# Performance work log

Measured on AMD Instinct MI355X. Metric: run time of the kernel, lower is better.

Reference implementation:

```python
import jax, jax.numpy as jnp
import numpy as np

B, C, T = 64, 22, 2560
U0, U1 = 128, 64  # lstm units per direction


def _lstm(x, Wx, Wh, b, reverse):
    """Keras-style LSTM. x:[B,T,D]. Returns (seq:[B,T,U], last:[B,U])."""
    if reverse:
        x = x[:, ::-1, :]
    U = Wh.shape[0]
    # precompute input projections for all timesteps: [T,B,4U]
    xz = (jnp.einsum('btd,dk->btk', x, Wx) + b).transpose(1, 0, 2)
    h0 = jnp.zeros((x.shape[0], U), x.dtype)
    c0 = jnp.zeros((x.shape[0], U), x.dtype)

    def step(carry, z):
        h, c = carry
        z = z + h @ Wh
        i = jax.nn.sigmoid(z[:, :U])
        f = jax.nn.sigmoid(z[:, U:2 * U])
        g = jnp.tanh(z[:, 2 * U:3 * U])
        o = jax.nn.sigmoid(z[:, 3 * U:])
        c = f * c + i * g
        h = o * jnp.tanh(c)
        return (h, c), h

    (h_last, _), hs = jax.lax.scan(step, (h0, c0), xz)
    hs = hs.transpose(1, 0, 2)  # [B,T,U]
    if reverse:
        hs = hs[:, ::-1, :]
    return hs, h_last


def setup_inputs() -> dict:
    key = jax.random.key(0)
    ks = jax.random.split(key, 20)
    s = 0.05
    d = {"x": jax.random.normal(ks[0], (B, C, T), jnp.float32)}
    # layer 0 (input dim C=22, units U0), fwd + bwd
    d["l0f_Wx"] = jax.random.normal(ks[1], (C, 4 * U0)) * s
    d["l0f_Wh"] = jax.random.normal(ks[2], (U0, 4 * U0)) * s
    d["l0f_b"] = jnp.zeros((4 * U0,))
    d["l0b_Wx"] = jax.random.normal(ks[3], (C, 4 * U0)) * s
    d["l0b_Wh"] = jax.random.normal(ks[4], (U0, 4 * U0)) * s
    d["l0b_b"] = jnp.zeros((4 * U0,))
    # layer 1 (input dim 2*U0=256, units U1), fwd + bwd
    d["l1f_Wx"] = jax.random.normal(ks[5], (2 * U0, 4 * U1)) * s
    d["l1f_Wh"] = jax.random.normal(ks[6], (U1, 4 * U1)) * s
    d["l1f_b"] = jnp.zeros((4 * U1,))
    d["l1b_Wx"] = jax.random.normal(ks[7], (2 * U0, 4 * U1)) * s
    d["l1b_Wh"] = jax.random.normal(ks[8], (U1, 4 * U1)) * s
    d["l1b_b"] = jnp.zeros((4 * U1,))
    # dense head: 2*U1=128 -> 128 -> 64 -> 1
    d["d0_W"] = jax.random.normal(ks[9], (2 * U1, 128)) * s
    d["d0_b"] = jnp.zeros((128,))
    d["d1_W"] = jax.random.normal(ks[10], (128, 64)) * s
    d["d1_b"] = jnp.zeros((64,))
    d["out_W"] = jax.random.normal(ks[11], (64, 1)) * s
    d["out_b"] = jnp.zeros((1,))
    return d


def reference(x, l0f_Wx, l0f_Wh, l0f_b, l0b_Wx, l0b_Wh, l0b_b,
              l1f_Wx, l1f_Wh, l1f_b, l1b_Wx, l1b_Wh, l1b_b,
              d0_W, d0_b, d1_W, d1_b, out_W, out_b):
    h = x.transpose(0, 2, 1)  # [B,T,C]
    # BiLSTM 0, return_sequences=True
    f_seq, _ = _lstm(h, l0f_Wx, l0f_Wh, l0f_b, reverse=False)
    b_seq, _ = _lstm(h, l0b_Wx, l0b_Wh, l0b_b, reverse=True)
    h = jnp.concatenate([f_seq, b_seq], axis=-1)  # [B,T,2*U0]
    # BiLSTM 1, return last state
    _, f_last = _lstm(h, l1f_Wx, l1f_Wh, l1f_b, reverse=False)
    _, b_last = _lstm(h, l1b_Wx, l1b_Wh, l1b_b, reverse=True)
    h = jnp.concatenate([f_last, b_last], axis=-1)  # [B,2*U1]
    # dense head (dropout inactive at inference)
    h = jax.nn.relu(h @ d0_W + d0_b)
    h = jax.nn.relu(h @ d1_W + d1_b)
    return jax.nn.sigmoid(h @ out_W + out_b)  # [B,1]
```

## Files before the change

### kernel.cpp

```cpp
#include <hip/hip_runtime.h>
#include <stdint.h>

#define TT 2560
#define BB 64
#define CC 22

typedef unsigned short ushort_t;
typedef __attribute__((ext_vector_type(4))) float floatx4;
typedef __attribute__((ext_vector_type(8))) short bf16x8;
typedef __attribute__((ext_vector_type(4))) int intx4;

__device__ __forceinline__ float bf2f(ushort_t u){
  union { uint32_t i; float f; } v; v.i = ((uint32_t)u) << 16; return v.f;
}
__device__ __forceinline__ ushort_t f2bf(float f){
  union { float f; uint32_t i; } v; v.f = f;
  uint32_t r = v.i + 0x7FFFu + ((v.i >> 16) & 1u);
  return (ushort_t)(r >> 16);
}
__device__ __forceinline__ float fsig(float x){ return 1.f/(1.f + __expf(-x)); }
__device__ __forceinline__ float ftanh(float x){ return 2.f/(1.f + __expf(-2.f*x)) - 1.f; }

__device__ __forceinline__ void ldsbar(){
  asm volatile("s_waitcnt lgkmcnt(0)\n\ts_barrier" ::: "memory");
}

__global__ __launch_bounds__(256) void k_convert_x(const float* __restrict__ x, ushort_t* __restrict__ xc){
  int i4 = blockIdx.x*256 + threadIdx.x;
  if (i4 >= BB*CC*TT/4) return;
  const float4 v = ((const float4*)x)[i4];
  uint2 o;
  o.x = (uint32_t)f2bf(v.x) | ((uint32_t)f2bf(v.y) << 16);
  o.y = (uint32_t)f2bf(v.z) | ((uint32_t)f2bf(v.w) << 16);
  ((uint2*)xc)[i4] = o;
}

__global__ __launch_bounds__(256) void k_prep_xa(const ushort_t* __restrict__ xc, ushort_t* __restrict__ xA){
  int idx = blockIdx.x*256 + threadIdx.x;
  if (idx >= 16*TT*16) return;
  int l16 = idx & 15;
  int rest = idx >> 4;
  int t = rest % TT, cb = rest / TT;
  int c4 = l16 >> 2, q = l16 & 3;
  int b = cb*4 + c4;
  ushort_t v[8];
  #pragma unroll
  for (int j=0;j<8;j++){
    int c = q*8 + j;
    v[j] = (c < CC) ? xc[((size_t)b*CC + c)*TT + t] : (ushort_t)0;
  }
  *(uint4*)(xA + (size_t)idx*8) = *(const uint4*)v;
}

__global__ __launch_bounds__(256) void k_wmax(const float* __restrict__ w0f, const float* __restrict__ w0b,
                                              const float* __restrict__ w1f, const float* __restrict__ w1b,
                                              float* __restrict__ scl){
  const int b = blockIdx.x;
  const float* W = (b==0) ? w0f : (b==1) ? w0b : (b==2) ? w1f : w1b;
  const int n = (b < 2) ? 128*512 : 64*256;
  float mx = 0.f;
  for (int i = threadIdx.x; i < n; i += 256) mx = fmaxf(mx, fabsf(W[i]));
  __shared__ float red[256];
  red[threadIdx.x] = mx;
  __syncthreads();
  for (int s = 128; s > 0; s >>= 1){
    if (threadIdx.x < s) red[threadIdx.x] = fmaxf(red[threadIdx.x], red[threadIdx.x+s]);
    __syncthreads();
  }
  if (threadIdx.x == 0) scl[b] = fmaxf(red[0], 1e-8f);
}

__global__ __launch_bounds__(256) void k_prep_l0(const float* __restrict__ WxF, const float* __restrict__ WhF,
                                                 const float* __restrict__ WxB, const float* __restrict__ WhB,
                                                 const float* __restrict__ scl,
                                                 char* __restrict__ W0Q, ushort_t* __restrict__ B0X){
  int idx = blockIdx.x*256 + threadIdx.x;
  if (idx >= 2*512*160) return;
  int dir = idx / 81920; int r = idx % 81920; int n = r / 160; int k = r % 160;
  if (k < 128){
    const float* Wh = dir ? WhB : WhF;
    float sw = scl[dir];
    W0Q[(size_t)dir*65536 + n*128 + k] = (char)(int)rintf(Wh[k*512 + n] * (127.f/sw));
  } else {
    const float* Wx = dir ? WxB : WxF;
    int kx = k - 128;
    float v = (kx < CC) ? Wx[kx*512 + n] : 0.f;
    B0X[(size_t)dir*16384 + n*32 + kx] = f2bf(v);
  }
}

__global__ __launch_bounds__(256) void k_prep_l1(const float* __restrict__ WhF, const float* __restrict__ WhB,
                                                 const float* __restrict__ scl,
                                                 char* __restrict__ W1Q){
  int idx = blockIdx.x*256 + threadIdx.x;
  if (idx >= 2*256*64) return;
  int dir = idx >> 14; int r = idx & 16383; int n = r >> 6; int k = r & 63;
  const float* Wh = dir ? WhB : WhF;
  float sw = scl[2+dir];
  W1Q[(size_t)dir*16384 + n*64 + k] = (char)(int)rintf(Wh[k*256 + n] * (127.f/sw));
}

__global__ __launch_bounds__(256) void k_prep_wxT(const float* __restrict__ Wf, const float* __restrict__ Wb,
                                                  ushort_t* __restrict__ WT){
  int idx = blockIdx.x*256 + threadIdx.x;
  int dir = idx >> 16; int r = idx & 65535; int n = r >> 8; int k = r & 255;
  const float* W = dir ? Wb : Wf;
  WT[idx] = f2bf(W[k*256 + n]);
}

__global__ __launch_bounds__(512, 2) void k_lstm0m(
  const ushort_t* __restrict__ xA, const char* __restrict__ W0Q,
  const ushort_t* __restrict__ B0X, const float* __restrict__ scl,
  const float* __restrict__ bF, const float* __restrict__ bB,
  ushort_t* __restrict__ h0seq)
{
  const int dir = blockIdx.x & 1, cb = blockIdx.x >> 1;
  const int tid = threadIdx.x;
  const int wv = tid >> 6, lane = tid & 63, m = lane & 15, q = lane >> 4;
  const int u = wv*16 + m;
  const float* bi = dir ? bB : bF;
  const float sclc = scl[dir] * (1.f/16129.f);

  __shared__ __align__(16) char AbufC[2][4][144];

  bf16x8 Bfx[4];
  intx4  BfQ[4][2];
  {
    const ushort_t* Bx = B0X + (size_t)dir*16384;
    const char*     Bq = W0Q + (size_t)dir*65536;
    #pragma unroll
    for (int g=0; g<4; g++){
      int nrow = (g*8 + wv)*16 + m;
      Bfx[g] = *(const bf16x8*)(Bx + (size_t)nrow*32 + q*8);
      #pragma unroll
      for (int kt=0; kt<2; kt++)
        BfQ[g][kt] = *(const intx4*)(Bq + (size_t)nrow*128 + kt*64 + q*16);
    }
  }
  float bz[4];
  #pragma unroll
  for (int g=0; g<4; g++) bz[g] = bi[g*128 + u];

  if (tid < (int)(sizeof(AbufC)/4)) ((uint32_t*)AbufC)[tid] = 0u;

  const ushort_t* xap = xA + (((size_t)cb*TT)*16 + (size_t)((m>>2)*4 + q))*8;
  uint4 px[4];
  #pragma unroll
  for (int j=0; j<4; j++){
    int tj = dir ? (TT-1-j) : j;
    px[j] = *(const uint4*)(xap + (size_t)tj*128);
  }
  const ushort_t* xpp = xap + (size_t)(dir ? (TT-5) : 4)*128;
  const int xstep = dir ? -128 : 128;
  __syncthreads();

  const floatx4 z4 = {0.f,0.f,0.f,0.f};
  const intx4  zi = {0,0,0,0};
  float cst = 0.f;
  const int t00 = dir ? TT-1 : 0;
  ushort_t* hp = h0seq + ((size_t)(cb*4 + q)*TT + t00)*256 + dir*128 + u;
  const int hstep = dir ? -256 : 256;

  const int ch = m >> 2;

  for (int i = 0; i < TT/4; ++i){
    #pragma unroll
    for (int p = 0; p < 4; ++p){
      const int s = i*4 + p;
      const int cur = s & 1, nxt = cur ^ 1;

      const char* ar = &AbufC[cur][ch][0];
      intx4 AfQ0 = *(const intx4*)(ar + q*16);
      intx4 AfQ1 = *(const intx4*)(ar + 64 + q*16);
      bf16x8 Ax = *(const bf16x8*)&px[p];

      floatx4 ax0 = __builtin_amdgcn_mfma_f32_16x16x32_bf16(Ax, Bfx[0], z4, 0,0,0);
      floatx4 ax1 = __builtin_amdgcn_mfma_f32_16x16x32_bf16(Ax, Bfx[1], z4, 0,0,0);
      floatx4 ax2 = __builtin_amdgcn_mfma_f32_16x16x32_bf16(Ax, Bfx[2], z4, 0,0,0);
      floatx4 ax3 = __builtin_amdgcn_mfma_f32_16x16x32_bf16(Ax, Bfx[3], z4, 0,0,0);

      intx4 aq0 = __builtin_amdgcn_mfma_i32_16x16x64_i8(AfQ0, BfQ[0][0], zi, 0,0,0);
      intx4 aq1 = __builtin_amdgcn_mfma_i32_16x16x64_i8(AfQ0, BfQ[1][0], zi, 0,0,0);
      intx4 aq2 = __builtin_amdgcn_mfma_i32_16x16x64_i8(AfQ0, BfQ[2][0], zi, 0,0,0);
      intx4 aq3 = __builtin_amdgcn_mfma_i32_16x16x64_i8(AfQ0, BfQ[3][0], zi, 0,0,0);
      aq0 = __builtin_amdgcn_mfma_i32_16x16x64_i8(AfQ1, BfQ[0][1], aq0, 0,0,0);
      aq1 = __builtin_amdgcn_mfma_i32_16x16x64_i8(AfQ1, BfQ[1][1], aq1, 0,0,0);
      aq2 = __builtin_amdgcn_mfma_i32_16x16x64_i8(AfQ1, BfQ[2][1], aq2, 0,0,0);
      aq3 = __builtin_amdgcn_mfma_i32_16x16x64_i8(AfQ1, BfQ[3][1], aq3, 0,0,0);

      px[p] = *(const uint4*)xpp;
      xpp += xstep;

      {
        float ig = fsig ((float)aq0[0]*sclc + ax0[0] + bz[0]);
        float fg = fsig ((float)aq1[0]*sclc + ax1[0] + bz[1]);
        float gg = ftanh((float)aq2[0]*sclc + ax2[0] + bz[2]);
        float og = fsig ((float)aq3[0]*sclc + ax3[0] + bz[3]);
        float cc = fg*cst + ig*gg;
        cst = cc;
        float hf = og*ftanh(cc);
        AbufC[nxt][q][u] = (char)(int)rintf(hf * 127.f);
        *hp = f2bf(hf); hp += hstep;
      }
      ldsbar();
    }
  }
}

__global__ __launch_bounds__(512) void k_xz1_gemm(const ushort_t* __restrict__ h0seq,
                                                  const ushort_t* __restrict__ WxT,
                                                  ushort_t* __restrict__ xz1)
{
  const int mb  = blockIdx.x;
  const int dir = blockIdx.y;
  const ushort_t* W   = WxT + (size_t)dir*256*256;
  ushort_t*       out = xz1 + (size_t)dir*BB*TT*256;
  const int wave = threadIdx.x >> 6;
  const int lane = threadIdx.x & 63;
  const int mw = wave & 3;
  const int nw = wave >> 2;
  const int m_ = lane & 15;
  const int q_ = lane >> 4;

  floatx4 acc[2][8];
  #pragma unroll
  for (int a=0;a<2;a++)
    #pragma unroll
    for (int n=0;n<8;n++) acc[a][n] = (floatx4)0.f;

  const size_t Abase = ((size_t)mb*128 + mw*32 + m_)*256 + q_*8;
  const size_t Bbase = ((size_t)nw*128 + m_)*256 + q_*8;

  for (int kc = 0; kc < 256; kc += 32){
    bf16x8 afr[2];
    #pragma unroll
    for (int mt=0;mt<2;mt++)
      afr[mt] = *(const bf16x8*)(h0seq + Abase + (size_t)mt*16*256 + kc);
    #pragma unroll
    for (int nt=0;nt<8;nt++){
      bf16x8 bfr = *(const bf16x8*)(W + Bbase + (size_t)nt*16*256 + kc);
      #pragma unroll
      for (int mt=0;mt<2;mt++)
        acc[mt][nt] = __builtin_amdgcn_mfma_f32_16x16x32_bf16(afr[mt], bfr, acc[mt][nt], 0,0,0);
    }
  }
  #pragma unroll
  for (int mt=0;mt<2;mt++)
    #pragma unroll
    for (int r=0;r<4;r++){
      size_t bt = (size_t)mb*128 + mw*32 + mt*16 + q_*4 + r;
      ushort_t* rowp = out + bt*256;
      #pragma unroll
      for (int wvz=0; wvz<4; wvz++){
        uint32_t lo = f2bf(acc[mt][wvz][r]);
        uint32_t hi = f2bf(acc[mt][wvz+4][r]);
        *(uint32_t*)(rowp + (wvz*16+m_)*4 + 2*nw) = lo | (hi << 16);
      }
    }
}

__global__ __launch_bounds__(256, 1) void k_lstm1m(
  const ushort_t* __restrict__ xz1R,
  const char* __restrict__ W1Q,
  const float* __restrict__ scl,
  const float* __restrict__ bF, const float* __restrict__ bB,
  float* __restrict__ h1last)
{
  const int dir = blockIdx.x & 1, cb = blockIdx.x >> 1;
  const int tid = threadIdx.x;
  const int wv = tid >> 6, lane = tid & 63, m = lane & 15, q = lane >> 4;
  const int u = wv*16 + m;
  const float* bi = dir ? bB : bF;
  const float sclc = scl[2+dir] * (1.f/16129.f);

  __shared__ __align__(16) char HbufC[2][4][80];

  intx4 BfQ[4];
  {
    const char* Bq = W1Q + (size_t)dir*16384;
    #pragma unroll
    for (int g=0; g<4; g++){
      int nrow = (g*4 + wv)*16 + m;
      BfQ[g] = *(const intx4*)(Bq + (size_t)nrow*64 + q*16);
    }
  }
  float bz[4];
  #pragma unroll
  for (int g=0; g<4; g++) bz[g] = bi[g*64 + u];

  if (tid < (int)(sizeof(HbufC)/4)) ((uint32_t*)HbufC)[tid] = 0u;

  const ushort_t* xzr = xz1R + ((size_t)dir*BB + (size_t)(cb*4+q))*TT*256 + (size_t)u*4;
  uint2 pz[4];
  #pragma unroll
  for (int j=0; j<4; j++){
    int tj = dir ? (TT-1-j) : j;
    pz[j] = *(const uint2*)(xzr + (size_t)tj*256);
  }
  const ushort_t* xpp = xzr + (size_t)(dir ? (TT-5) : 4)*256;
  const int zstep = dir ? -256 : 256;
  __syncthreads();

  const intx4 zi = {0,0,0,0};
  float cst = 0.f, hl = 0.f;
  const int ch = m >> 2;

  for (int i = 0; i < TT/4; ++i){
    #pragma unroll
    for (int p = 0; p < 4; ++p){
      const int s = i*4 + p;
      const int cur = s & 1, nxt = cur ^ 1;

      intx4 AfQ = *(const intx4*)(&HbufC[cur][ch][0] + q*16);

      float w0 = bz[0] + bf2f((ushort_t)(pz[p].x & 0xffff));
      float w1 = bz[1] + bf2f((ushort_t)(pz[p].x >> 16));
      float w2 = bz[2] + bf2f((ushort_t)(pz[p].y & 0xffff));
      float w3 = bz[3] + bf2f((ushort_t)(pz[p].y >> 16));
      pz[p] = *(const uint2*)xpp;
      xpp += zstep;

      intx4 a0 = __builtin_amdgcn_mfma_i32_16x16x64_i8(AfQ, BfQ[0], zi, 0,0,0);
      intx4 a1 = __builtin_amdgcn_mfma_i32_16x16x64_i8(AfQ, BfQ[1], zi, 0,0,0);
      intx4 a2 = __builtin_amdgcn_mfma_i32_16x16x64_i8(AfQ, BfQ[2], zi, 0,0,0);
      intx4 a3 = __builtin_amdgcn_mfma_i32_16x16x64_i8(AfQ, BfQ[3], zi, 0,0,0);

      {
        float ig = fsig((float)a0[0]*sclc + w0);
        float fg = fsig((float)a1[0]*sclc + w1);
        float gg = ftanh((float)a2[0]*sclc + w2);
        float og = fsig((float)a3[0]*sclc + w3);
        float cc = fg*cst + ig*gg;
        cst = cc;
        hl = og*ftanh(cc);
        HbufC[nxt][q][u] = (char)(int)rintf(hl * 127.f);
      }
      ldsbar();
    }
  }
  h1last[(size_t)(cb*4 + q)*128 + dir*64 + u] = hl;
}

__global__ __launch_bounds__(128) void k_head(
  const float* __restrict__ h1last,
  const float* __restrict__ d0W, const float* __restrict__ d0b,
  const float* __restrict__ d1W, const float* __restrict__ d1b,
  const float* __restrict__ oW,  const float* __restrict__ ob,
  float* __restrict__ outp)
{
  const int b = blockIdx.x;
  const int j = threadIdx.x;
  __shared__ float v0[128], v1[128];
  v0[j] = h1last[b*128 + j];
  __syncthreads();
  float acc = d0b[j];
  #pragma unroll
  for (int k=0;k<128;k++) acc += v0[k]*d0W[k*128 + j];
  v1[j] = fmaxf(acc, 0.f);
  __syncthreads();
  if (j < 64){
    float a2 = d1b[j];
    #pragma unroll
    for (int k=0;k<128;k++) a2 += v1[k]*d1W[k*64 + j];
    float p = fmaxf(a2, 0.f) * oW[j];
    #pragma unroll
    for (int off=32; off>0; off>>=1) p += __shfl_down(p, off, 64);
    if (j == 0) outp[b] = 1.f/(1.f + __expf(-(p + ob[0])));
  }
}

extern "C" void kernel_launch(void* const* d_in, const int* in_sizes, int n_in,
                              void* d_out, int out_size, void* d_ws, size_t ws_size,
                              hipStream_t stream)
{
  const float* x     = (const float*)d_in[0];
  const float* l0fWx = (const float*)d_in[1];
  const float* l0fWh = (const float*)d_in[2];
  const float* l0fb  = (const float*)d_in[3];
  const float* l0bWx = (const float*)d_in[4];
  const float* l0bWh = (const float*)d_in[5];
  const float* l0bb  = (const float*)d_in[6];
  const float* l1fWx = (const float*)d_in[7];
  const float* l1fWh = (const float*)d_in[8];
  const float* l1fb  = (const float*)d_in[9];
  const float* l1bWx = (const float*)d_in[10];
  const float* l1bWh = (const float*)d_in[11];
  const float* l1bb  = (const float*)d_in[12];
  const float* d0W = (const float*)d_in[13];
  const float* d0b = (const float*)d_in[14];
  const float* d1W = (const float*)d_in[15];
  const float* d1b = (const float*)d_in[16];
  const float* oW  = (const float*)d_in[17];
  const float* ob  = (const float*)d_in[18];
  float* outp = (float*)d_out;

  char* ws = (char*)d_ws;
  const size_t OFF_XT  = 0;
  const size_t OFF_SCL = 7208960ull;
  const size_t OFF_H0  = OFF_XT  + 7864320ull;
  const size_t OFF_XZ  = OFF_H0  + 83886080ull;
  const size_t OFF_XA  = OFF_XZ;
  const size_t OFF_WT  = OFF_XZ  + 167772160ull;
  const size_t OFF_B0  = OFF_WT  + 262144ull;
  const size_t OFF_B0X = OFF_B0  + 131072ull;
  const size_t OFF_B1  = OFF_B0  + 327680ull;
  const size_t OFF_H1  = OFF_B1  + 65536ull;

  ushort_t* xc  = (ushort_t*)(ws + OFF_XT);
  float*    sclp= (float*)(ws + OFF_SCL);
  ushort_t* h0  = (ushort_t*)(ws + OFF_H0);
  ushort_t* xz1 = (ushort_t*)(ws + OFF_XZ);
  ushort_t* xA  = (ushort_t*)(ws + OFF_XA);
  ushort_t* WT  = (ushort_t*)(ws + OFF_WT);
  char*     W0Q = (char*)(ws + OFF_B0);
  ushort_t* B0X = (ushort_t*)(ws + OFF_B0X);
  char*     W1Q = (char*)(ws + OFF_B1);
  float*    h1l = (float*)(ws + OFF_H1);

  hipLaunchKernelGGL(k_convert_x,   dim3(3520), dim3(256), 0, stream, x, xc);
  hipLaunchKernelGGL(k_prep_xa,     dim3(2560), dim3(256), 0, stream, xc, xA);
  hipLaunchKernelGGL(k_wmax,        dim3(4),    dim3(256), 0, stream, l0fWh, l0bWh, l1fWh, l1bWh, sclp);
  hipLaunchKernelGGL(k_prep_l0,     dim3(640),  dim3(256), 0, stream, l0fWx, l0fWh, l0bWx, l0bWh, sclp, W0Q, B0X);
  hipLaunchKernelGGL(k_prep_l1,     dim3(128),  dim3(256), 0, stream, l1fWh, l1bWh, sclp, W1Q);
  hipLaunchKernelGGL(k_prep_wxT,    dim3(512),  dim3(256), 0, stream, l1fWx, l1bWx, WT);
  hipLaunchKernelGGL(k_lstm0m,      dim3(32),   dim3(512), 0, stream, xA, W0Q, B0X, sclp, l0fb, l0bb, h0);
  hipLaunchKernelGGL(k_xz1_gemm,    dim3(1280,2), dim3(512), 0, stream, h0, WT, xz1);
  hipLaunchKernelGGL(k_lstm1m,      dim3(32),   dim3(256), 0, stream, xz1, W1Q, sclp, l1fb, l1bb, h1l);
  hipLaunchKernelGGL(k_head,        dim3(64),   dim3(128), 0, stream,
                     h1l, d0W, d0b, d1W, d1b, oW, ob, outp);
}
```

Measured before the change: 2.514 ms.

## Run layer-1 LSTM with one wave per batch/direction, dropping block barriers

```diff
diff --git a/kernel.cpp b/kernel.cpp
--- a/kernel.cpp
+++ b/kernel.cpp
@@ -23,6 +23,9 @@
 
 __device__ __forceinline__ void ldsbar(){
   asm volatile("s_waitcnt lgkmcnt(0)\n\ts_barrier" ::: "memory");
+}
+__device__ __forceinline__ void ldsfence(){
+  asm volatile("s_waitcnt lgkmcnt(0)" ::: "memory");
 }
 
 __global__ __launch_bounds__(256) void k_convert_x(const float* __restrict__ x, ushort_t* __restrict__ xc){
@@ -259,38 +262,39 @@
     }
 }
 
-__global__ __launch_bounds__(256, 1) void k_lstm1m(
+__global__ __launch_bounds__(64, 1) void k_lstm1m(
   const ushort_t* __restrict__ xz1R,
   const char* __restrict__ W1Q,
   const float* __restrict__ scl,
   const float* __restrict__ bF, const float* __restrict__ bB,
   float* __restrict__ h1last)
 {
-  const int dir = blockIdx.x & 1, cb = blockIdx.x >> 1;
-  const int tid = threadIdx.x;
-  const int wv = tid >> 6, lane = tid & 63, m = lane & 15, q = lane >> 4;
-  const int u = wv*16 + m;
+  const int dir = blockIdx.x & 1, b = blockIdx.x >> 1;
+  const int lane = threadIdx.x;
+  const int m = lane & 15, q = lane >> 4;
+  const int u = q*16 + m;
   const float* bi = dir ? bB : bF;
   const float sclc = scl[2+dir] * (1.f/16129.f);
-
-  __shared__ __align__(16) char HbufC[2][4][80];
-
-  intx4 BfQ[4];
+  const bool qodd = (q & 1), qhi = (q >= 2);
+
+  __shared__ __align__(16) char hbuf[128];
+
+  intx4 BfQ[4][4];
   {
     const char* Bq = W1Q + (size_t)dir*16384;
     #pragma unroll
-    for (int g=0; g<4; g++){
-      int nrow = (g*4 + wv)*16 + m;
-      BfQ[g] = *(const intx4*)(Bq + (size_t)nrow*64 + q*16);
-    }
+    for (int g=0; g<4; g++)
+      #pragma unroll
+      for (int ut=0; ut<4; ut++)
+        BfQ[g][ut] = *(const intx4*)(Bq + (size_t)(g*64 + ut*16 + m)*64 + q*16);
   }
   float bz[4];
   #pragma unroll
   for (int g=0; g<4; g++) bz[g] = bi[g*64 + u];
 
-  if (tid < (int)(sizeof(HbufC)/4)) ((uint32_t*)HbufC)[tid] = 0u;
-
-  const ushort_t* xzr = xz1R + ((size_t)dir*BB + (size_t)(cb*4+q))*TT*256 + (size_t)u*4;
+  if (lane < 32) ((uint32_t*)hbuf)[lane] = 0u;
+
+  const ushort_t* xzr = xz1R + ((size_t)dir*BB + b)*TT*256 + (size_t)u*4;
   uint2 pz[4];
   #pragma unroll
   for (int j=0; j<4; j++){
@@ -299,19 +303,15 @@
   }
   const ushort_t* xpp = xzr + (size_t)(dir ? (TT-5) : 4)*256;
   const int zstep = dir ? -256 : 256;
-  __syncthreads();
+  ldsfence();
 
   const intx4 zi = {0,0,0,0};
   float cst = 0.f, hl = 0.f;
-  const int ch = m >> 2;
 
   for (int i = 0; i < TT/4; ++i){
     #pragma unroll
     for (int p = 0; p < 4; ++p){
-      const int s = i*4 + p;
-      const int cur = s & 1, nxt = cur ^ 1;
-
-      intx4 AfQ = *(const intx4*)(&HbufC[cur][ch][0] + q*16);
+      intx4 AfQ = *(const intx4*)(hbuf + q*16);
 
       float w0 = bz[0] + bf2f((ushort_t)(pz[p].x & 0xffff));
       float w1 = bz[1] + bf2f((ushort_t)(pz[p].x >> 16));
@@ -320,25 +320,32 @@
       pz[p] = *(const uint2*)xpp;
       xpp += zstep;
 
-      intx4 a0 = __builtin_amdgcn_mfma_i32_16x16x64_i8(AfQ, BfQ[0], zi, 0,0,0);
-      intx4 a1 = __builtin_amdgcn_mfma_i32_16x16x64_i8(AfQ, BfQ[1], zi, 0,0,0);
-      intx4 a2 = __builtin_amdgcn_mfma_i32_16x16x64_i8(AfQ, BfQ[2], zi, 0,0,0);
-      intx4 a3 = __builtin_amdgcn_mfma_i32_16x16x64_i8(AfQ, BfQ[3], zi, 0,0,0);
+      intx4 C[4][4];
+      #pragma unroll
+      for (int g=0; g<4; g++)
+        #pragma unroll
+        for (int ut=0; ut<4; ut++)
+          C[g][ut] = __builtin_amdgcn_mfma_i32_16x16x64_i8(AfQ, BfQ[g][ut], zi, 0,0,0);
+
+      int z0i = qhi ? (qodd ? C[0][3][0] : C[0][2][0]) : (qodd ? C[0][1][0] : C[0][0][0]);
+      int z1i = qhi ? (qodd ? C[1][3][0] : C[1][2][0]) : (qodd ? C[1][1][0] : C[1][0][0]);
+      int z2i = qhi ? (qodd ? C[2][3][0] : C[2][2][0]) : (qodd ? C[2][1][0] : C[2][0][0]);
+      int z3i = qhi ? (qodd ? C[3][3][0] : C[3][2][0]) : (qodd ? C[3][1][0] : C[3][0][0]);
 
       {
-        float ig = fsig((float)a0[0]*sclc + w0);
-        float fg = fsig((float)a1[0]*sclc + w1);
-        float gg = ftanh((float)a2[0]*sclc + w2);
-        float og = fsig((float)a3[0]*sclc + w3);
+        float ig = fsig((float)z0i*sclc + w0);
+        float fg = fsig((float)z1i*sclc + w1);
+        float gg = ftanh((float)z2i*sclc + w2);
+        float og = fsig((float)z3i*sclc + w3);
         float cc = fg*cst + ig*gg;
         cst = cc;
         hl = og*ftanh(cc);
-        HbufC[nxt][q][u] = (char)(int)rintf(hl * 127.f);
+        hbuf[u] = (char)(int)rintf(hl * 127.f);
       }
-      ldsbar();
+      ldsfence();
     }
   }
-  h1last[(size_t)(cb*4 + q)*128 + dir*64 + u] = hl;
+  h1last[(size_t)b*128 + dir*64 + u] = hl;
 }
 
 __global__ __launch_bounds__(128) void k_head(
@@ -425,7 +432,7 @@
   hipLaunchKernelGGL(k_prep_wxT,    dim3(512),  dim3(256), 0, stream, l1fWx, l1bWx, WT);
   hipLaunchKernelGGL(k_lstm0m,      dim3(32),   dim3(512), 0, stream, xA, W0Q, B0X, sclp, l0fb, l0bb, h0);
   hipLaunchKernelGGL(k_xz1_gemm,    dim3(1280,2), dim3(512), 0, stream, h0, WT, xz1);
-  hipLaunchKernelGGL(k_lstm1m,      dim3(32),   dim3(256), 0, stream, xz1, W1Q, sclp, l1fb, l1bb, h1l);
+  hipLaunchKernelGGL(k_lstm1m,      dim3(128),  dim3(64), 0, stream, xz1, W1Q, sclp, l1fb, l1bb, h1l);
   hipLaunchKernelGGL(k_head,        dim3(64),   dim3(128), 0, stream,
                      h1l, d0W, d0b, d1W, d1b, oW, ob, outp);
 }
```

New measurement: 2.737 ms. 1.09x slower.

## Split layer-0 LSTM to one batch row per block with gate-per-lane activation

Applied to the files above, without the earlier changes.

```diff
diff --git a/kernel.cpp b/kernel.cpp
--- a/kernel.cpp
+++ b/kernel.cpp
@@ -37,12 +37,10 @@
 
 __global__ __launch_bounds__(256) void k_prep_xa(const ushort_t* __restrict__ xc, ushort_t* __restrict__ xA){
   int idx = blockIdx.x*256 + threadIdx.x;
-  if (idx >= 16*TT*16) return;
-  int l16 = idx & 15;
-  int rest = idx >> 4;
-  int t = rest % TT, cb = rest / TT;
-  int c4 = l16 >> 2, q = l16 & 3;
-  int b = cb*4 + c4;
+  if (idx >= BB*TT*4) return;
+  int q = idx & 3;
+  int rest = idx >> 2;
+  int t = rest % TT, b = rest / TT;
   ushort_t v[8];
   #pragma unroll
   for (int j=0;j<8;j++){
@@ -76,16 +74,19 @@
                                                  char* __restrict__ W0Q, ushort_t* __restrict__ B0X){
   int idx = blockIdx.x*256 + threadIdx.x;
   if (idx >= 2*512*160) return;
-  int dir = idx / 81920; int r = idx % 81920; int n = r / 160; int k = r % 160;
+  int dir = idx / 81920; int r0 = idx % 81920; int n = r0 / 160; int k = r0 % 160;
+  int g = n >> 7, u = n & 127;
+  int wv = u >> 4, qq = (u >> 2) & 3, r = u & 3;
+  int row = (qq*8 + wv)*16 + (r*4 + g);
   if (k < 128){
     const float* Wh = dir ? WhB : WhF;
     float sw = scl[dir];
-    W0Q[(size_t)dir*65536 + n*128 + k] = (char)(int)rintf(Wh[k*512 + n] * (127.f/sw));
+    W0Q[(size_t)dir*65536 + row*128 + k] = (char)(int)rintf(Wh[k*512 + n] * (127.f/sw));
   } else {
     const float* Wx = dir ? WxB : WxF;
     int kx = k - 128;
     float v = (kx < CC) ? Wx[kx*512 + n] : 0.f;
-    B0X[(size_t)dir*16384 + n*32 + kx] = f2bf(v);
+    B0X[(size_t)dir*16384 + row*32 + kx] = f2bf(v);
   }
 }
 
@@ -108,20 +109,25 @@
   WT[idx] = f2bf(W[k*256 + n]);
 }
 
-__global__ __launch_bounds__(512, 2) void k_lstm0m(
+__global__ __launch_bounds__(512, 1) void k_lstm0m(
   const ushort_t* __restrict__ xA, const char* __restrict__ W0Q,
   const ushort_t* __restrict__ B0X, const float* __restrict__ scl,
   const float* __restrict__ bF, const float* __restrict__ bB,
   ushort_t* __restrict__ h0seq)
 {
-  const int dir = blockIdx.x & 1, cb = blockIdx.x >> 1;
+  const int dir = blockIdx.x & 1, b = blockIdx.x >> 1;
   const int tid = threadIdx.x;
   const int wv = tid >> 6, lane = tid & 63, m = lane & 15, q = lane >> 4;
-  const int u = wv*16 + m;
+  const int g  = m & 3;
+  const int u  = wv*16 + q*4 + (m >> 2);
   const float* bi = dir ? bB : bF;
   const float sclc = scl[dir] * (1.f/16129.f);
-
-  __shared__ __align__(16) char AbufC[2][4][144];
+  const float em = (g==2) ? -2.f : -1.f;
+  const float ym = (g==2) ?  2.f :  1.f;
+  const float ya = (g==2) ? -1.f :  0.f;
+  const float bzl = bi[g*128 + u];
+
+  __shared__ __align__(16) char AbufC[2][128];
 
   bf16x8 Bfx[4];
   intx4  BfQ[4][2];
@@ -129,39 +135,34 @@
     const ushort_t* Bx = B0X + (size_t)dir*16384;
     const char*     Bq = W0Q + (size_t)dir*65536;
     #pragma unroll
-    for (int g=0; g<4; g++){
-      int nrow = (g*8 + wv)*16 + m;
-      Bfx[g] = *(const bf16x8*)(Bx + (size_t)nrow*32 + q*8);
+    for (int qt=0; qt<4; qt++){
+      int nrow = (qt*8 + wv)*16 + m;
+      Bfx[qt] = *(const bf16x8*)(Bx + (size_t)nrow*32 + q*8);
       #pragma unroll
       for (int kt=0; kt<2; kt++)
-        BfQ[g][kt] = *(const intx4*)(Bq + (size_t)nrow*128 + kt*64 + q*16);
-    }
-  }
-  float bz[4];
-  #pragma unroll
-  for (int g=0; g<4; g++) bz[g] = bi[g*128 + u];
-
-  if (tid < (int)(sizeof(AbufC)/4)) ((uint32_t*)AbufC)[tid] = 0u;
-
-  const ushort_t* xap = xA + (((size_t)cb*TT)*16 + (size_t)((m>>2)*4 + q))*8;
+        BfQ[qt][kt] = *(const intx4*)(Bq + (size_t)nrow*128 + kt*64 + q*16);
+    }
+  }
+
+  if (tid < 64) ((uint32_t*)AbufC)[tid] = 0u;
+
+  const ushort_t* xap = xA + ((size_t)b*TT*4 + q)*8;
   uint4 px[4];
   #pragma unroll
   for (int j=0; j<4; j++){
     int tj = dir ? (TT-1-j) : j;
-    px[j] = *(const uint4*)(xap + (size_t)tj*128);
-  }
-  const ushort_t* xpp = xap + (size_t)(dir ? (TT-5) : 4)*128;
-  const int xstep = dir ? -128 : 128;
+    px[j] = *(const uint4*)(xap + (size_t)tj*32);
+  }
+  const ushort_t* xpp = xap + (size_t)(dir ? (TT-5) : 4)*32;
+  const int xstep = dir ? -32 : 32;
   __syncthreads();
 
   const floatx4 z4 = {0.f,0.f,0.f,0.f};
   const intx4  zi = {0,0,0,0};
   float cst = 0.f;
   const int t00 = dir ? TT-1 : 0;
-  ushort_t* hp = h0seq + ((size_t)(cb*4 + q)*TT + t00)*256 + dir*128 + u;
+  ushort_t* hp = h0seq + ((size_t)b*TT + t00)*256 + dir*128 + u;
   const int hstep = dir ? -256 : 256;
-
-  const int ch = m >> 2;
 
   for (int i = 0; i < TT/4; ++i){
     #pragma unroll
@@ -169,7 +170,7 @@
       const int s = i*4 + p;
       const int cur = s & 1, nxt = cur ^ 1;
 
-      const char* ar = &AbufC[cur][ch][0];
+      const char* ar = &AbufC[cur][0];
       intx4 AfQ0 = *(const intx4*)(ar + q*16);
       intx4 AfQ1 = *(const intx4*)(ar + 64 + q*16);
       bf16x8 Ax = *(const bf16x8*)&px[p];
@@ -191,16 +192,30 @@
       px[p] = *(const uint4*)xpp;
       xpp += xstep;
 
+      float axs = (q < 2) ? ((q == 0) ? ax0[0] : ax1[0])
+                          : ((q == 2) ? ax2[0] : ax3[0]);
+      int   aqs = (q < 2) ? ((q == 0) ? aq0[0] : aq1[0])
+                          : ((q == 2) ? aq2[0] : aq3[0]);
+
       {
-        float ig = fsig ((float)aq0[0]*sclc + ax0[0] + bz[0]);
-        float fg = fsig ((float)aq1[0]*sclc + ax1[0] + bz[1]);
-        float gg = ftanh((float)aq2[0]*sclc + ax2[0] + bz[2]);
-        float og = fsig ((float)aq3[0]*sclc + ax3[0] + bz[3]);
-        float cc = fg*cst + ig*gg;
+        float z = (float)aqs*sclc + axs + bzl;
+        float e = __expf(z * em);
+        float y = 1.f/(1.f + e);
+        float act = ym*y + ya;
+
+        int ai = __float_as_int(act);
+        float sf = __int_as_float(__builtin_amdgcn_ds_swizzle(ai, 0x041F));
+        float sg = __int_as_float(__builtin_amdgcn_ds_swizzle(ai, 0x081F));
+        float so = __int_as_float(__builtin_amdgcn_ds_swizzle(ai, 0x0C1F));
+
+        float cc = sf*cst + act*sg;
         cst = cc;
-        float hf = og*ftanh(cc);
-        AbufC[nxt][q][u] = (char)(int)rintf(hf * 127.f);
-        *hp = f2bf(hf); hp += hstep;
+        float hl = so*ftanh(cc);
+        if (g == 0){
+          AbufC[nxt][u] = (char)(int)rintf(hl * 127.f);
+          *hp = f2bf(hl);
+        }
+        hp += hstep;
       }
       ldsbar();
     }
@@ -423,7 +438,7 @@
   hipLaunchKernelGGL(k_prep_l0,     dim3(640),  dim3(256), 0, stream, l0fWx, l0fWh, l0bWx, l0bWh, sclp, W0Q, B0X);
   hipLaunchKernelGGL(k_prep_l1,     dim3(128),  dim3(256), 0, stream, l1fWh, l1bWh, sclp, W1Q);
   hipLaunchKernelGGL(k_prep_wxT,    dim3(512),  dim3(256), 0, stream, l1fWx, l1bWx, WT);
-  hipLaunchKernelGGL(k_lstm0m,      dim3(32),   dim3(512), 0, stream, xA, W0Q, B0X, sclp, l0fb, l0bb, h0);
+  hipLaunchKernelGGL(k_lstm0m,      dim3(128),  dim3(512), 0, stream, xA, W0Q, B0X, sclp, l0fb, l0bb, h0);
   hipLaunchKernelGGL(k_xz1_gemm,    dim3(1280,2), dim3(512), 0, stream, h0, WT, xz1);
   hipLaunchKernelGGL(k_lstm1m,      dim3(32),   dim3(256), 0, stream, xz1, W1Q, sclp, l1fb, l1bb, h1l);
   hipLaunchKernelGGL(k_head,        dim3(64),   dim3(128), 0, stream,
```

Result: faster. 2.131 ms (-15.2%).
